# Performance work log

Measured on AMD Instinct MI355X. Metric: run time of the kernel, lower is better.

Reference implementation:

```python
import jax, jax.numpy as jnp
import numpy as np

N_SUPPORT = 4096
N_QUERY = 8192
H = W = 28
IN_DIM = H * W  # 784
EMBED_DIM = 512
N_CLASSES = 64


def setup_inputs() -> dict:
    key = jax.random.key(0)
    k1, k2, k3, k4 = jax.random.split(key, 4)
    support_set = jax.random.normal(k1, (N_SUPPORT, 1, H, W), dtype=jnp.float32)
    query_set = jax.random.normal(k2, (N_QUERY, 1, H, W), dtype=jnp.float32)
    # one-hot support labels (N, C)
    lbl = jax.random.randint(k3, (N_SUPPORT,), 0, N_CLASSES)
    support_labels = jax.nn.one_hot(lbl, N_CLASSES, dtype=jnp.float32)
    # encoder params: flatten + dense projection stand-in for embedding_net
    W_enc = jax.random.normal(k4, (IN_DIM, EMBED_DIM), dtype=jnp.float32) * (1.0 / np.sqrt(IN_DIM))
    b_enc = jnp.zeros((EMBED_DIM,), dtype=jnp.float32)
    return {
        "support_set": support_set,
        "query_set": query_set,
        "support_labels": support_labels,
        "W_enc": W_enc,
        "b_enc": b_enc,
    }


def _encode(x, W_enc, b_enc):
    # (B, 1, H, W) -> (B, D): flatten + linear projection
    B = x.shape[0]
    return x.reshape(B, -1) @ W_enc + b_enc


def _neg_cdist(q, s):
    # -euclidean distance, computed via the expansion ||q-s||^2 = |q|^2 + |s|^2 - 2 q.s
    q2 = jnp.sum(q * q, axis=-1, keepdims=True)          # (Q, 1)
    s2 = jnp.sum(s * s, axis=-1)[None, :]                # (1, N)
    qs = jnp.einsum("qd,nd->qn", q, s)                  # (Q, N)
    d2 = jnp.maximum(q2 + s2 - 2.0 * qs, 0.0)
    return -jnp.sqrt(d2)


def reference(support_set, query_set, support_labels, W_enc, b_enc):
    support_emb = _encode(support_set, W_enc, b_enc)     # (N, D)
    query_emb = _encode(query_set, W_enc, b_enc)         # (Q, D)
    distances = _neg_cdist(query_emb, support_emb)       # (Q, N)
    attention = jax.nn.softmax(distances, axis=1)        # (Q, N)
    predictions = attention @ support_labels             # (Q, C)
    return predictions
```

## Files before the change

### kernel.cpp

```cpp
#include <hip/hip_runtime.h>

#define N_SUP 4096
#define N_QRY 8192
#define IN_DIM 784
#define EMB 512
#define NCLS 64
#define M_TOT (N_SUP + N_QRY)

typedef _Float16 f16;
typedef _Float16 f16x8 __attribute__((ext_vector_type(8)));
typedef float f32x4 __attribute__((ext_vector_type(4)));

static __device__ __forceinline__ f16x8 cvt8(const float* p) {
    float4 a = *(const float4*)p;
    float4 b = *(const float4*)(p + 4);
    f16x8 v;
    v[0] = (f16)a.x; v[1] = (f16)a.y; v[2] = (f16)a.z; v[3] = (f16)a.w;
    v[4] = (f16)b.x; v[5] = (f16)b.y; v[6] = (f16)b.z; v[7] = (f16)b.w;
    return v;
}

__global__ __launch_bounds__(256) void prep_wt(const float* __restrict__ W,
                                               f16* __restrict__ WT) {
    __shared__ float T[32][33];
    const int k0 = blockIdx.x * 32, n0 = blockIdx.y * 32;
    const int tx = threadIdx.x & 31, ty = threadIdx.x >> 5;
#pragma unroll
    for (int i = 0; i < 4; ++i) {
        int k = k0 + ty + i * 8;
        T[ty + i * 8][tx] = (k < IN_DIM) ? W[(size_t)k * EMB + n0 + tx] : 0.f;
    }
    __syncthreads();
#pragma unroll
    for (int i = 0; i < 4; ++i) {
        int n = n0 + ty + i * 8;
        int k = k0 + tx;
        if (k < IN_DIM) WT[(size_t)n * IN_DIM + k] = (f16)T[tx][ty + i * 8];
    }
}

__global__ void prep_lbl(const float* __restrict__ lab, int* __restrict__ lbl) {
    int s = blockIdx.x * 256 + threadIdx.x;
    if (s >= N_SUP) return;
    int best = 0; float bv = -1e30f;
    for (int c = 0; c < NCLS; ++c) {
        float v = lab[s * NCLS + c];
        if (v > bv) { bv = v; best = c; }
    }
    lbl[s] = best;
}

__global__ void prep_L(const int* __restrict__ lbl, f16* __restrict__ Lcs) {
    int idx = blockIdx.x * 256 + threadIdx.x;
    if (idx >= NCLS * N_SUP) return;
    int c = idx >> 12, s = idx & (N_SUP - 1);
    Lcs[idx] = (lbl[s] == c) ? (f16)1.f : (f16)0.f;
}

__global__ __launch_bounds__(256) void encode(
    const float* __restrict__ sup, const float* __restrict__ qry,
    const f16* __restrict__ WT, const float* __restrict__ bias,
    f16* __restrict__ E, float* __restrict__ norms)
{
    __shared__ __align__(16) f16 Xs[128][40];
    __shared__ __align__(16) f16 Ws[64][40];
    const int tid = threadIdx.x;
    const int w = tid >> 6, lane = tid & 63;
    const int q = lane >> 4, c16 = lane & 15;
    const int m0 = blockIdx.x * 128, n0 = blockIdx.y * 64;

    f32x4 acc[2][4];
#pragma unroll
    for (int h = 0; h < 2; ++h)
#pragma unroll
        for (int nb = 0; nb < 4; ++nb) acc[h][nb] = (f32x4){0.f, 0.f, 0.f, 0.f};

    const int sr = tid >> 2;
    const int koff = (tid & 3) * 8;
    const float *xrow0, *xrow1;
    {
        int g0 = m0 + sr, g1 = m0 + sr + 64;
        xrow0 = (g0 < N_SUP) ? sup + (size_t)g0 * IN_DIM : qry + (size_t)(g0 - N_SUP) * IN_DIM;
        xrow1 = (g1 < N_SUP) ? sup + (size_t)g1 * IN_DIM : qry + (size_t)(g1 - N_SUP) * IN_DIM;
    }
    const f16* wrow = WT + (size_t)(n0 + sr) * IN_DIM;

    for (int k0 = 0; k0 < IN_DIM; k0 += 32) {
        __syncthreads();
        if (k0 + koff + 8 <= IN_DIM) {
            *(f16x8*)&Xs[sr][koff]      = cvt8(xrow0 + k0 + koff);
            *(f16x8*)&Xs[sr + 64][koff] = cvt8(xrow1 + k0 + koff);
            *(f16x8*)&Ws[sr][koff]      = *(const f16x8*)(wrow + k0 + koff);
        } else {
            f16x8 z = (f16x8){0,0,0,0,0,0,0,0};
            *(f16x8*)&Xs[sr][koff]      = z;
            *(f16x8*)&Xs[sr + 64][koff] = z;
            *(f16x8*)&Ws[sr][koff]      = z;
        }
        __syncthreads();
        f16x8 a0 = *(const f16x8*)&Xs[w * 16 + c16][q * 8];
        f16x8 a1 = *(const f16x8*)&Xs[64 + w * 16 + c16][q * 8];
#pragma unroll
        for (int nb = 0; nb < 4; ++nb) {
            f16x8 b = *(const f16x8*)&Ws[nb * 16 + c16][q * 8];
            acc[0][nb] = __builtin_amdgcn_mfma_f32_16x16x32_f16(a0, b, acc[0][nb], 0, 0, 0);
            acc[1][nb] = __builtin_amdgcn_mfma_f32_16x16x32_f16(a1, b, acc[1][nb], 0, 0, 0);
        }
    }

    float nrm[2][4] = {};
#pragma unroll
    for (int nb = 0; nb < 4; ++nb) {
        int col = n0 + nb * 16 + c16;
        float bv = bias[col];
#pragma unroll
        for (int h = 0; h < 2; ++h)
#pragma unroll
            for (int r = 0; r < 4; ++r) {
                int row = m0 + h * 64 + w * 16 + q * 4 + r;
                float v = acc[h][nb][r] + bv;
                E[(size_t)row * EMB + col] = (f16)v;
                nrm[h][r] += v * v;
            }
    }
#pragma unroll
    for (int h = 0; h < 2; ++h)
#pragma unroll
        for (int r = 0; r < 4; ++r) {
            float v = nrm[h][r];
            v += __shfl_xor(v, 1); v += __shfl_xor(v, 2);
            v += __shfl_xor(v, 4); v += __shfl_xor(v, 8);
            if (c16 == 0) atomicAdd(&norms[m0 + h * 64 + w * 16 + q * 4 + r], v);
        }
}

__global__ __launch_bounds__(256) void anchor(const f16* __restrict__ E,
                                              const float* __restrict__ norms,
                                              float* __restrict__ manc) {
    __shared__ float s0e[EMB];
    const int tid = threadIdx.x;
    s0e[tid] = (float)E[tid];
    s0e[tid + 256] = (float)E[tid + 256];
    __syncthreads();
    const int qrow = blockIdx.x * 256 + tid;
    const f16* qp = E + (size_t)(N_SUP + qrow) * EMB;
    float dot = 0.f;
    for (int k = 0; k < EMB; k += 8) {
        f16x8 v = *(const f16x8*)(qp + k);
#pragma unroll
        for (int j = 0; j < 8; ++j) dot += (float)v[j] * s0e[k + j];
    }
    float d2 = fmaxf(norms[N_SUP + qrow] + norms[0] - 2.f * dot, 0.f);
    manc[qrow] = sqrtf(d2);
}

__global__ __launch_bounds__(256, 3) void attn(
    const f16* __restrict__ E, const float* __restrict__ norms,
    const float* __restrict__ manc, const f16* __restrict__ Lcs,
    float* __restrict__ Num)
{
    __shared__ __align__(16) f16 Ss[2][64][136];
    __shared__ __align__(16) f16 Pt[4][16][72];
    const int tid = threadIdx.x;
    const int w = tid >> 6, lane = tid & 63;
    const int q = lane >> 4, c16 = lane & 15;
    const int qt = blockIdx.x, ss = blockIdx.y;

    f16x8 qf[16];
    const f16* qb = E + (size_t)(N_SUP + qt * 64 + w * 16 + c16) * EMB + q * 8;
#pragma unroll
    for (int ks = 0; ks < 16; ++ks) qf[ks] = *(const f16x8*)(qb + ks * 32);
    float q2[4], mrow[4];
#pragma unroll
    for (int r = 0; r < 4; ++r) {
        q2[r]   = norms[N_SUP + qt * 64 + w * 16 + q * 4 + r];
        mrow[r] = manc[qt * 64 + w * 16 + q * 4 + r];
    }

    f32x4 accPL[4];
#pragma unroll
    for (int nb = 0; nb < 4; ++nb) accPL[nb] = (f32x4){0.f, 0.f, 0.f, 0.f};

    const int sr = tid >> 2, koff0 = (tid & 3) * 8;
    const f16* sbase = E + (size_t)(ss * 512 + sr) * EMB;

    f16x8 g[4];
#pragma unroll
    for (int i = 0; i < 4; ++i) g[i] = *(const f16x8*)(sbase + koff0 + i * 32);
#pragma unroll
    for (int i = 0; i < 4; ++i) *(f16x8*)&Ss[0][sr][koff0 + i * 32] = g[i];
    __syncthreads();

    for (int it = 0; it < 8; ++it) {
        f32x4 accQK[4];
#pragma unroll
        for (int nb = 0; nb < 4; ++nb) accQK[nb] = (f32x4){0.f, 0.f, 0.f, 0.f};
#pragma unroll
        for (int kc = 0; kc < 4; ++kc) {
            const int idx = it * 4 + kc;
            const int cur = idx & 1;
            if (idx + 1 < 32) {
                const int nit = (idx + 1) >> 2, nkc = (idx + 1) & 3;
                const f16* src = sbase + (size_t)(nit * 64) * EMB + nkc * 128 + koff0;
#pragma unroll
                for (int i = 0; i < 4; ++i) g[i] = *(const f16x8*)(src + i * 32);
            }
#pragma unroll
            for (int ksl = 0; ksl < 4; ++ksl) {
#pragma unroll
                for (int nb = 0; nb < 4; ++nb) {
                    f16x8 b = *(const f16x8*)&Ss[cur][nb * 16 + c16][ksl * 32 + q * 8];
                    accQK[nb] = __builtin_amdgcn_mfma_f32_16x16x32_f16(qf[kc * 4 + ksl], b, accQK[nb], 0, 0, 0);
                }
            }
            if (idx + 1 < 32) {
#pragma unroll
                for (int i = 0; i < 4; ++i) *(f16x8*)&Ss[cur ^ 1][sr][koff0 + i * 32] = g[i];
            }
            __syncthreads();
        }
        const int s0g = ss * 512 + it * 64;
#pragma unroll
        for (int nb = 0; nb < 4; ++nb) {
            const int col = s0g + nb * 16 + c16;
            const float s2 = norms[col];
#pragma unroll
            for (int r = 0; r < 4; ++r) {
                float d2 = fmaxf(q2[r] + s2 - 2.f * accQK[nb][r], 0.f);
                float p = __expf(mrow[r] - sqrtf(d2));
                p = fminf(p, 60000.f);
                Pt[w][q * 4 + r][nb * 16 + c16] = (f16)p;
            }
        }
#pragma unroll
        for (int kc2 = 0; kc2 < 2; ++kc2) {
            f16x8 af = *(const f16x8*)&Pt[w][c16][kc2 * 32 + q * 8];
#pragma unroll
            for (int nbc = 0; nbc < 4; ++nbc) {
                f16x8 bl = *(const f16x8*)(Lcs + (size_t)(nbc * 16 + c16) * N_SUP + s0g + kc2 * 32 + q * 8);
                accPL[nbc] = __builtin_amdgcn_mfma_f32_16x16x32_f16(af, bl, accPL[nbc], 0, 0, 0);
            }
        }
    }
#pragma unroll
    for (int nbc = 0; nbc < 4; ++nbc)
#pragma unroll
        for (int r = 0; r < 4; ++r)
            atomicAdd(&Num[(size_t)(qt * 64 + w * 16 + q * 4 + r) * NCLS + nbc * 16 + c16],
                      accPL[nbc][r]);
}

__global__ __launch_bounds__(256) void finalize(const float* __restrict__ Num,
                                                float* __restrict__ out) {
    const int tid = threadIdx.x;
    const int w = tid >> 6, lane = tid & 63;
    const int qrow = blockIdx.x * 4 + w;
    float v = Num[(size_t)qrow * NCLS + lane];
    float s = v;
    s += __shfl_xor(s, 1);  s += __shfl_xor(s, 2);  s += __shfl_xor(s, 4);
    s += __shfl_xor(s, 8);  s += __shfl_xor(s, 16); s += __shfl_xor(s, 32);
    out[(size_t)qrow * NCLS + lane] = v / s;
}

extern "C" void kernel_launch(void* const* d_in, const int* in_sizes, int n_in,
                              void* d_out, int out_size, void* d_ws, size_t ws_size,
                              hipStream_t stream) {
    (void)in_sizes; (void)n_in; (void)out_size; (void)ws_size;
    const float* sup  = (const float*)d_in[0];
    const float* qry  = (const float*)d_in[1];
    const float* lab  = (const float*)d_in[2];
    const float* Wenc = (const float*)d_in[3];
    const float* benc = (const float*)d_in[4];
    float* out = (float*)d_out;

    char* ws = (char*)d_ws;
    size_t off = 0;
    f16* WT = (f16*)(ws + off);        off += (size_t)EMB * IN_DIM * 2;
    f16* E  = (f16*)(ws + off);        off += (size_t)M_TOT * EMB * 2;
    float* norms = (float*)(ws + off); off += (size_t)M_TOT * 4;
    int* lbl = (int*)(ws + off);       off += (size_t)N_SUP * 4;
    f16* Lcs = (f16*)(ws + off);       off += (size_t)NCLS * N_SUP * 2;
    float* manc = (float*)(ws + off);  off += (size_t)N_QRY * 4;
    float* Num = (float*)(ws + off);   off += (size_t)N_QRY * NCLS * 4;

    hipMemsetAsync(norms, 0, (size_t)M_TOT * 4, stream);
    hipMemsetAsync(Num, 0, (size_t)N_QRY * NCLS * 4, stream);

    prep_wt<<<dim3(25, 16), 256, 0, stream>>>(Wenc, WT);
    prep_lbl<<<(N_SUP + 255) / 256, 256, 0, stream>>>(lab, lbl);
    prep_L<<<(NCLS * N_SUP + 255) / 256, 256, 0, stream>>>(lbl, Lcs);
    encode<<<dim3(M_TOT / 128, EMB / 64), 256, 0, stream>>>(sup, qry, WT, benc, E, norms);
    anchor<<<N_QRY / 256, 256, 0, stream>>>(E, norms, manc);
    attn<<<dim3(N_QRY / 64, 8), 256, 0, stream>>>(E, norms, manc, Lcs, Num);
    finalize<<<N_QRY / 4, 256, 0, stream>>>(Num, out);
}
```

Measured before the change: 236.8 us.

## Restructure encoder GEMM with MFMA-fragment-packed weights and full-row output tiles

Replaces the weight transpose with a pre-packing kernel that lays W out in MFMA B-fragment order, so encode loads weights straight from global/L2 into registers instead of staging them in LDS. Each encode block now computes 64 rows across all 512 columns, which means the input activations are read and converted only once rather than eight times, and the next input chunk is prefetched into registers. Row norms are reduced in shared memory and written directly, which removes the norms memset and the global atomics. The two label prep kernels are merged into one. Each wave now holds 32 accumulator vectors, which raises register pressure and may reduce occupancy, and the grid has fewer blocks.

After: 261.6 us. 1.11x slower.

```diff
diff --git a/kernel.cpp b/kernel.cpp
--- a/kernel.cpp
+++ b/kernel.cpp
@@ -6,6 +6,7 @@
 #define EMB 512
 #define NCLS 64
 #define M_TOT (N_SUP + N_QRY)
+#define NCHUNK 25
 
 typedef _Float16 f16;
 typedef _Float16 f16x8 __attribute__((ext_vector_type(8)));
@@ -20,26 +21,26 @@
     return v;
 }
 
-__global__ __launch_bounds__(256) void prep_wt(const float* __restrict__ W,
-                                               f16* __restrict__ WT) {
-    __shared__ float T[32][33];
-    const int k0 = blockIdx.x * 32, n0 = blockIdx.y * 32;
-    const int tx = threadIdx.x & 31, ty = threadIdx.x >> 5;
-#pragma unroll
-    for (int i = 0; i < 4; ++i) {
-        int k = k0 + ty + i * 8;
-        T[ty + i * 8][tx] = (k < IN_DIM) ? W[(size_t)k * EMB + n0 + tx] : 0.f;
-    }
-    __syncthreads();
-#pragma unroll
-    for (int i = 0; i < 4; ++i) {
-        int n = n0 + ty + i * 8;
-        int k = k0 + tx;
-        if (k < IN_DIM) WT[(size_t)n * IN_DIM + k] = (f16)T[tx][ty + i * 8];
-    }
-}
-
-__global__ void prep_lbl(const float* __restrict__ lab, int* __restrict__ lbl) {
+__global__ __launch_bounds__(256) void prep_wb(const float* __restrict__ W,
+                                               f16* __restrict__ Wb) {
+    int g = blockIdx.x * 256 + threadIdx.x;
+    if (g >= NCHUNK * 32 * 64) return;
+    int chunk = g >> 11;
+    int rem = g & 2047;
+    int nbg = rem >> 6, lane = rem & 63;
+    int n = nbg * 16 + (lane & 15);
+    int kbase = chunk * 32 + (lane >> 4) * 8;
+    f16x8 v;
+#pragma unroll
+    for (int j = 0; j < 8; ++j) {
+        int k = kbase + j;
+        v[j] = (k < IN_DIM) ? (f16)W[(size_t)k * EMB + n] : (f16)0.f;
+    }
+    *(f16x8*)(Wb + (size_t)g * 8) = v;
+}
+
+__global__ __launch_bounds__(256) void prep_labels(const float* __restrict__ lab,
+                                                   f16* __restrict__ Lcs) {
     int s = blockIdx.x * 256 + threadIdx.x;
     if (s >= N_SUP) return;
     int best = 0; float bv = -1e30f;
@@ -47,62 +48,60 @@
         float v = lab[s * NCLS + c];
         if (v > bv) { bv = v; best = c; }
     }
-    lbl[s] = best;
-}
-
-__global__ void prep_L(const int* __restrict__ lbl, f16* __restrict__ Lcs) {
-    int idx = blockIdx.x * 256 + threadIdx.x;
-    if (idx >= NCLS * N_SUP) return;
-    int c = idx >> 12, s = idx & (N_SUP - 1);
-    Lcs[idx] = (lbl[s] == c) ? (f16)1.f : (f16)0.f;
+#pragma unroll
+    for (int c = 0; c < NCLS; ++c)
+        Lcs[(size_t)c * N_SUP + s] = (c == best) ? (f16)1.f : (f16)0.f;
 }
 
 __global__ __launch_bounds__(256) void encode(
     const float* __restrict__ sup, const float* __restrict__ qry,
-    const f16* __restrict__ WT, const float* __restrict__ bias,
+    const f16* __restrict__ Wb, const float* __restrict__ bias,
     f16* __restrict__ E, float* __restrict__ norms)
 {
-    __shared__ __align__(16) f16 Xs[128][40];
-    __shared__ __align__(16) f16 Ws[64][40];
+    __shared__ __align__(16) f16 Xs[64][40];
+    __shared__ float normS[64];
     const int tid = threadIdx.x;
     const int w = tid >> 6, lane = tid & 63;
     const int q = lane >> 4, c16 = lane & 15;
-    const int m0 = blockIdx.x * 128, n0 = blockIdx.y * 64;
-
-    f32x4 acc[2][4];
+    const int m0 = blockIdx.x * 64;
+    const int rbase = (w & 1) * 32;
+    const int cbase = (w >> 1) * 256;
+    const int nbg0 = (w >> 1) * 16;
+
+    f32x4 acc[2][16];
 #pragma unroll
     for (int h = 0; h < 2; ++h)
 #pragma unroll
-        for (int nb = 0; nb < 4; ++nb) acc[h][nb] = (f32x4){0.f, 0.f, 0.f, 0.f};
+        for (int nb = 0; nb < 16; ++nb) acc[h][nb] = (f32x4){0.f, 0.f, 0.f, 0.f};
+
+    if (tid < 64) normS[tid] = 0.f;
 
     const int sr = tid >> 2;
-    const int koff = (tid & 3) * 8;
-    const float *xrow0, *xrow1;
+    const int sq = tid & 3;
+    const float* xrow;
     {
-        int g0 = m0 + sr, g1 = m0 + sr + 64;
-        xrow0 = (g0 < N_SUP) ? sup + (size_t)g0 * IN_DIM : qry + (size_t)(g0 - N_SUP) * IN_DIM;
-        xrow1 = (g1 < N_SUP) ? sup + (size_t)g1 * IN_DIM : qry + (size_t)(g1 - N_SUP) * IN_DIM;
-    }
-    const f16* wrow = WT + (size_t)(n0 + sr) * IN_DIM;
-
-    for (int k0 = 0; k0 < IN_DIM; k0 += 32) {
+        int gr = m0 + sr;
+        xrow = (gr < N_SUP) ? sup + (size_t)gr * IN_DIM
+                            : qry + (size_t)(gr - N_SUP) * IN_DIM;
+    }
+
+    f16x8 xg = cvt8(xrow + sq * 8);
+
+    for (int c = 0; c < NCHUNK; ++c) {
         __syncthreads();
-        if (k0 + koff + 8 <= IN_DIM) {
-            *(f16x8*)&Xs[sr][koff]      = cvt8(xrow0 + k0 + koff);
-            *(f16x8*)&Xs[sr + 64][koff] = cvt8(xrow1 + k0 + koff);
-            *(f16x8*)&Ws[sr][koff]      = *(const f16x8*)(wrow + k0 + koff);
-        } else {
-            f16x8 z = (f16x8){0,0,0,0,0,0,0,0};
-            *(f16x8*)&Xs[sr][koff]      = z;
-            *(f16x8*)&Xs[sr + 64][koff] = z;
-            *(f16x8*)&Ws[sr][koff]      = z;
-        }
+        *(f16x8*)&Xs[sr][sq * 8] = xg;
         __syncthreads();
-        f16x8 a0 = *(const f16x8*)&Xs[w * 16 + c16][q * 8];
-        f16x8 a1 = *(const f16x8*)&Xs[64 + w * 16 + c16][q * 8];
-#pragma unroll
-        for (int nb = 0; nb < 4; ++nb) {
-            f16x8 b = *(const f16x8*)&Ws[nb * 16 + c16][q * 8];
+        if (c + 1 < NCHUNK) {
+            int k = (c + 1) * 32 + sq * 8;
+            if (k + 8 <= IN_DIM) xg = cvt8(xrow + k);
+            else xg = (f16x8){0,0,0,0,0,0,0,0};
+        }
+        f16x8 a0 = *(const f16x8*)&Xs[rbase + c16][q * 8];
+        f16x8 a1 = *(const f16x8*)&Xs[rbase + 16 + c16][q * 8];
+        const f16* wb = Wb + ((size_t)(c * 32 + nbg0) * 64 + lane) * 8;
+#pragma unroll
+        for (int nb = 0; nb < 16; ++nb) {
+            f16x8 b = *(const f16x8*)(wb + (size_t)nb * 512);
             acc[0][nb] = __builtin_amdgcn_mfma_f32_16x16x32_f16(a0, b, acc[0][nb], 0, 0, 0);
             acc[1][nb] = __builtin_amdgcn_mfma_f32_16x16x32_f16(a1, b, acc[1][nb], 0, 0, 0);
         }
@@ -110,16 +109,16 @@
 
     float nrm[2][4] = {};
 #pragma unroll
-    for (int nb = 0; nb < 4; ++nb) {
-        int col = n0 + nb * 16 + c16;
+    for (int nb = 0; nb < 16; ++nb) {
+        int col = cbase + nb * 16 + c16;
         float bv = bias[col];
 #pragma unroll
         for (int h = 0; h < 2; ++h)
 #pragma unroll
             for (int r = 0; r < 4; ++r) {
-                int row = m0 + h * 64 + w * 16 + q * 4 + r;
+                int rowl = rbase + h * 16 + q * 4 + r;
                 float v = acc[h][nb][r] + bv;
-                E[(size_t)row * EMB + col] = (f16)v;
+                E[(size_t)(m0 + rowl) * EMB + col] = (f16)v;
                 nrm[h][r] += v * v;
             }
     }
@@ -130,8 +129,10 @@
             float v = nrm[h][r];
             v += __shfl_xor(v, 1); v += __shfl_xor(v, 2);
             v += __shfl_xor(v, 4); v += __shfl_xor(v, 8);
-            if (c16 == 0) atomicAdd(&norms[m0 + h * 64 + w * 16 + q * 4 + r], v);
-        }
+            if (c16 == 0) atomicAdd(&normS[rbase + h * 16 + q * 4 + r], v);
+        }
+    __syncthreads();
+    if (tid < 64) norms[m0 + tid] = normS[tid];
 }
 
 __global__ __launch_bounds__(256) void anchor(const f16* __restrict__ E,
@@ -275,21 +276,18 @@
 
     char* ws = (char*)d_ws;
     size_t off = 0;
-    f16* WT = (f16*)(ws + off);        off += (size_t)EMB * IN_DIM * 2;
+    f16* Wb = (f16*)(ws + off);        off += (size_t)NCHUNK * 32 * 64 * 8 * 2;
     f16* E  = (f16*)(ws + off);        off += (size_t)M_TOT * EMB * 2;
     float* norms = (float*)(ws + off); off += (size_t)M_TOT * 4;
-    int* lbl = (int*)(ws + off);       off += (size_t)N_SUP * 4;
     f16* Lcs = (f16*)(ws + off);       off += (size_t)NCLS * N_SUP * 2;
     float* manc = (float*)(ws + off);  off += (size_t)N_QRY * 4;
     float* Num = (float*)(ws + off);   off += (size_t)N_QRY * NCLS * 4;
 
-    hipMemsetAsync(norms, 0, (size_t)M_TOT * 4, stream);
     hipMemsetAsync(Num, 0, (size_t)N_QRY * NCLS * 4, stream);
 
-    prep_wt<<<dim3(25, 16), 256, 0, stream>>>(Wenc, WT);
-    prep_lbl<<<(N_SUP + 255) / 256, 256, 0, stream>>>(lab, lbl);
-    prep_L<<<(NCLS * N_SUP + 255) / 256, 256, 0, stream>>>(lbl, Lcs);
-    encode<<<dim3(M_TOT / 128, EMB / 64), 256, 0, stream>>>(sup, qry, WT, benc, E, norms);
+    prep_wb<<<(NCHUNK * 32 * 64 + 255) / 256, 256, 0, stream>>>(Wenc, Wb);
+    prep_labels<<<N_SUP / 256, 256, 0, stream>>>(lab, Lcs);
+    encode<<<M_TOT / 64, 256, 0, stream>>>(sup, qry, Wb, benc, E, norms);
     anchor<<<N_QRY / 256, 256, 0, stream>>>(E, norms, manc);
     attn<<<dim3(N_QRY / 64, 8), 256, 0, stream>>>(E, norms, manc, Lcs, Num);
     finalize<<<N_QRY / 4, 256, 0, stream>>>(Num, out);
```
